# Performance work log

Hardware: AMD Instinct MI355X
Metric: run time of the kernel (lower is better)

Reference implementation:

```python
import jax, jax.numpy as jnp
import numpy as np

T = 4096          # batch_size (time points)
C = 4096          # input_dims[1] == num_filters (channels/neurons)
FW = 64           # filter_width (temporal taps)


def setup_inputs() -> dict:
    key = jax.random.key(0)
    k1, k2, k3 = jax.random.split(key, 3)
    inputs = jax.random.normal(k1, (T, C), dtype=jnp.float32)
    weights = jax.random.uniform(k2, (FW, C), dtype=jnp.float32)
    biases = jax.random.normal(k3, (C,), dtype=jnp.float32) * 0.01
    return {"inputs": inputs, "weights": weights, "biases": biases}


def reference(inputs, weights, biases):
    # weight-norm (normalize_weights=1): per-filter L2 over taps, floored at 1e-8
    wnorms = jnp.maximum(jnp.sqrt(jnp.sum(jnp.square(weights), axis=0)), 1e-8)  # [C]
    filt = jnp.maximum(0.0, weights / wnorms)  # pos_constraint clamp, [FW, C]
    # Original does a full conv2d -> [C, T, 1, C] then takes the diagonal over
    # (batch-channel, filter-channel). Mathematically this is a per-channel
    # depthwise temporal SAME conv (cross-correlation, matching tf.nn.conv2d).
    x = inputs.T[None, :, :]            # [1, C, T]  (NCH)
    k = filt.T[:, None, :]              # [C, 1, FW] (OIH), group size 1
    pre = jax.lax.conv_general_dilated(
        x, k, window_strides=(1,), padding="SAME",
        feature_group_count=C,
        dimension_numbers=("NCH", "OIH", "NCH"))  # [1, C, T]
    # bias add; activation 'lin' = identity; ei_mask is None (num_inh=0)
    out = pre[0].T + biases[None, :]    # [T, C]
    return out
```

## Files before the change

### kernel.cpp

```cpp
#include <hip/hip_runtime.h>


#define T_DIM 4096
#define C_DIM 4096
#define PAD_L 31
#define HT    32
#define KTILE 128
#define NPER  (KTILE / 32)

template <bool GUARD>
__device__ __forceinline__ void fir_body(const float* __restrict__ x,
                                         const float* __restrict__ w,
                                         const float* __restrict__ b,
                                         float* __restrict__ out,
                                         int c, int half, int t0) {
    const float* __restrict__ xp = x + c;
    const float* __restrict__ wp = w + half * HT * C_DIM + c;
    float* __restrict__ opl = out + ((long long)t0 + half) * C_DIM + c;

    float wf[HT];
    float ss = 0.0f;
#pragma unroll
    for (int j = 0; j < HT; ++j) {
        wf[j] = wp[j * C_DIM];
        ss = fmaf(wf[j], wf[j], ss);
    }
    ss += __shfl_xor(ss, 32);
    const float inv = 1.0f / fmaxf(sqrtf(ss), 1e-8f);
#pragma unroll
    for (int j = 0; j < HT; ++j) wf[j] = fmaxf(wf[j] * inv, 0.0f);

    const float bv = b[c];
    const float se = (half == 0) ? bv : 0.0f;
    const float so = (half == 0) ? 0.0f : bv;

    const int base = t0 - PAD_L + HT * half;

    float xbuf[HT];
#pragma unroll
    for (int i = 0; i < HT; ++i) {
        const int m = base + i;
        float v = 0.0f;
        if (!GUARD || ((unsigned)m < (unsigned)T_DIM)) v = xp[(long long)m * C_DIM];
        xbuf[(1 + i) & 31] = v;
    }

    float pfA[16], pfB[16];
#pragma unroll
    for (int i = 0; i < 16; ++i) {
        const int m = base + 32 + i;
        float v = 0.0f;
        if (!GUARD || ((unsigned)m < (unsigned)T_DIM)) v = xp[(long long)m * C_DIM];
        pfA[i] = v;
    }
#pragma unroll
    for (int i = 0; i < 16; ++i) {
        const int m = base + 48 + i;
        float v = 0.0f;
        if (!GUARD || ((unsigned)m < (unsigned)T_DIM)) v = xp[(long long)m * C_DIM];
        pfB[i] = v;
    }

#define PARTIAL(kk, seed, dst)                                                \
    float dst;                                                                \
    {                                                                         \
        float a0 = (seed), a1 = 0.0f;                                         \
        _Pragma("unroll")                                                     \
        for (int j = 0; j < HT; j += 2) {                                     \
            a0 = fmaf(wf[j],     xbuf[((kk) + j + 1) & 31], a0);              \
            a1 = fmaf(wf[j + 1], xbuf[((kk) + j + 2) & 31], a1);              \
        }                                                                     \
        dst = a0 + a1;                                                        \
    }

#define STEP_PAIR(kk)                                                         \
    {                                                                         \
        PARTIAL(kk, se, pe)                                                   \
        xbuf[((kk) + 1) & 31] = ((kk) < 16) ? pfA[(kk) & 15] : pfB[(kk) & 15];\
        PARTIAL((kk) + 1, so, po)                                             \
        xbuf[((kk) + 2) & 31] =                                               \
            (((kk) + 1) < 16) ? pfA[((kk) + 1) & 15] : pfB[((kk) + 1) & 15];  \
        const float snd = (half == 0) ? po : pe;                              \
        const float rcv = __shfl_xor(snd, 32);                                \
        const float res = ((half == 0) ? pe : po) + rcv;                      \
        __builtin_nontemporal_store(res, opl + (long long)(kb + (kk)) * C_DIM);\
    }

#pragma unroll 1
    for (int p = 0; p < NPER; ++p) {
        const int kb = p * 32;
        STEP_PAIR(0)  STEP_PAIR(2)  STEP_PAIR(4)  STEP_PAIR(6)
        STEP_PAIR(8)  STEP_PAIR(10) STEP_PAIR(12) STEP_PAIR(14)
        if (p < NPER - 1) {
#pragma unroll
            for (int i = 0; i < 16; ++i) {
                const int m = base + 64 + kb + i;
                float v = 0.0f;
                if (!GUARD || ((unsigned)m < (unsigned)T_DIM)) v = xp[(long long)m * C_DIM];
                pfA[i] = v;
            }
        }
        STEP_PAIR(16) STEP_PAIR(18) STEP_PAIR(20) STEP_PAIR(22)
        STEP_PAIR(24) STEP_PAIR(26) STEP_PAIR(28) STEP_PAIR(30)
        if (p < NPER - 1) {
#pragma unroll
            for (int i = 0; i < 16; ++i) {
                const int m = base + 80 + kb + i;
                float v = 0.0f;
                if (!GUARD || ((unsigned)m < (unsigned)T_DIM)) v = xp[(long long)m * C_DIM];
                pfB[i] = v;
            }
        }
    }

#undef STEP_PAIR
#undef PARTIAL
}

__global__ __launch_bounds__(256)
__attribute__((amdgpu_waves_per_eu(3, 4)))
void depthwise_fir_kernel(const float* __restrict__ x, const float* __restrict__ w,
                          const float* __restrict__ b, float* __restrict__ out) {
    const int lane = threadIdx.x & 63;
    const int wave = threadIdx.x >> 6;
    const int c    = blockIdx.y * 128 + wave * 32 + (lane & 31);
    const int half = lane >> 5;
    const int t0   = blockIdx.x * KTILE;
    if (blockIdx.x == 0 || blockIdx.x == gridDim.x - 1)
        fir_body<true>(x, w, b, out, c, half, t0);
    else
        fir_body<false>(x, w, b, out, c, half, t0);
}

extern "C" void kernel_launch(void* const* d_in, const int* in_sizes, int n_in,
                              void* d_out, int out_size, void* d_ws, size_t ws_size,
                              hipStream_t stream) {
    const float* x = (const float*)d_in[0];
    const float* w = (const float*)d_in[1];
    const float* b = (const float*)d_in[2];
    float* out = (float*)d_out;

    dim3 grid(T_DIM / KTILE, C_DIM / 128);
    dim3 block(256);
    hipLaunchKernelGGL(depthwise_fir_kernel, grid, block, 0, stream, x, w, b, out);
}
```

Measured before the change: 50.38 us.

## Split filter taps across four lane groups to cut per-thread registers

Each filter's 64 taps are now split across four 16-lane groups instead of two 32-lane halves. Each thread holds 16 weights and a 16-entry input ring buffer, and partial sums are combined with two cross-lane shuffles per output. A wave now covers 16 channels instead of 32, the grid doubles along channels, and the waves-per-EU hint is removed. The aim is lower register pressure and higher occupancy, at the cost of more shuffles per output and narrower 64-byte row segments per load and store, which may hurt coalescing.

New measurement: 61.75 us. 1.23x slower.

```diff
diff --git a/kernel.cpp b/kernel.cpp
--- a/kernel.cpp
+++ b/kernel.cpp
@@ -4,108 +4,102 @@
 #define T_DIM 4096
 #define C_DIM 4096
 #define PAD_L 31
-#define HT    32
+#define QT    16
 #define KTILE 128
-#define NPER  (KTILE / 32)
+#define NPER  (KTILE / 16)
 
 template <bool GUARD>
 __device__ __forceinline__ void fir_body(const float* __restrict__ x,
                                          const float* __restrict__ w,
                                          const float* __restrict__ b,
                                          float* __restrict__ out,
-                                         int c, int half, int t0) {
+                                         int c, int grp, int t0) {
     const float* __restrict__ xp = x + c;
-    const float* __restrict__ wp = w + half * HT * C_DIM + c;
-    float* __restrict__ opl = out + ((long long)t0 + half) * C_DIM + c;
+    const float* __restrict__ wp = w + grp * QT * C_DIM + c;
 
-    float wf[HT];
+    float wf[QT];
     float ss = 0.0f;
 #pragma unroll
-    for (int j = 0; j < HT; ++j) {
+    for (int j = 0; j < QT; ++j) {
         wf[j] = wp[j * C_DIM];
         ss = fmaf(wf[j], wf[j], ss);
     }
+    ss += __shfl_xor(ss, 16);
     ss += __shfl_xor(ss, 32);
     const float inv = 1.0f / fmaxf(sqrtf(ss), 1e-8f);
 #pragma unroll
-    for (int j = 0; j < HT; ++j) wf[j] = fmaxf(wf[j] * inv, 0.0f);
+    for (int j = 0; j < QT; ++j) wf[j] = fmaxf(wf[j] * inv, 0.0f);
 
-    const float bv = b[c];
-    const float se = (half == 0) ? bv : 0.0f;
-    const float so = (half == 0) ? 0.0f : bv;
+    const float seed = (grp == 0) ? b[c] : 0.0f;
 
-    const int base = t0 - PAD_L + HT * half;
+    const int base = t0 - PAD_L + QT * grp;
 
-    float xbuf[HT];
+    float xbuf[QT];
 #pragma unroll
-    for (int i = 0; i < HT; ++i) {
+    for (int i = 0; i < QT; ++i) {
         const int m = base + i;
         float v = 0.0f;
         if (!GUARD || ((unsigned)m < (unsigned)T_DIM)) v = xp[(long long)m * C_DIM];
-        xbuf[(1 + i) & 31] = v;
+        xbuf[(1 + i) & 15] = v;
     }
 
-    float pfA[16], pfB[16];
+    float pfA[8], pfB[8];
 #pragma unroll
-    for (int i = 0; i < 16; ++i) {
-        const int m = base + 32 + i;
+    for (int i = 0; i < 8; ++i) {
+        const int m = base + QT + i;
         float v = 0.0f;
         if (!GUARD || ((unsigned)m < (unsigned)T_DIM)) v = xp[(long long)m * C_DIM];
         pfA[i] = v;
     }
 #pragma unroll
-    for (int i = 0; i < 16; ++i) {
-        const int m = base + 48 + i;
+    for (int i = 0; i < 8; ++i) {
+        const int m = base + QT + 8 + i;
         float v = 0.0f;
         if (!GUARD || ((unsigned)m < (unsigned)T_DIM)) v = xp[(long long)m * C_DIM];
         pfB[i] = v;
     }
 
-#define PARTIAL(kk, seed, dst)                                                \
-    float dst;                                                                \
+    float res = 0.0f;
+    float* __restrict__ opl = out + ((long long)t0 + grp) * C_DIM + c;
+
+#define FIR_STEP(kk, src)                                                     \
     {                                                                         \
-        float a0 = (seed), a1 = 0.0f;                                         \
+        float a0 = seed, a1 = 0.0f;                                           \
         _Pragma("unroll")                                                     \
-        for (int j = 0; j < HT; j += 2) {                                     \
-            a0 = fmaf(wf[j],     xbuf[((kk) + j + 1) & 31], a0);              \
-            a1 = fmaf(wf[j + 1], xbuf[((kk) + j + 2) & 31], a1);              \
+        for (int j = 0; j < QT; j += 2) {                                     \
+            a0 = fmaf(wf[j],     xbuf[((kk) + j + 1) & 15], a0);              \
+            a1 = fmaf(wf[j + 1], xbuf[((kk) + j + 2) & 15], a1);              \
         }                                                                     \
-        dst = a0 + a1;                                                        \
-    }
-
-#define STEP_PAIR(kk)                                                         \
-    {                                                                         \
-        PARTIAL(kk, se, pe)                                                   \
-        xbuf[((kk) + 1) & 31] = ((kk) < 16) ? pfA[(kk) & 15] : pfB[(kk) & 15];\
-        PARTIAL((kk) + 1, so, po)                                             \
-        xbuf[((kk) + 2) & 31] =                                               \
-            (((kk) + 1) < 16) ? pfA[((kk) + 1) & 15] : pfB[((kk) + 1) & 15];  \
-        const float snd = (half == 0) ? po : pe;                              \
-        const float rcv = __shfl_xor(snd, 32);                                \
-        const float res = ((half == 0) ? pe : po) + rcv;                      \
-        __builtin_nontemporal_store(res, opl + (long long)(kb + (kk)) * C_DIM);\
+        xbuf[((kk) + 1) & 15] = src[(kk) & 7];                                \
+        float p1 = a0 + a1;                                                   \
+        p1 += __shfl_xor(p1, 16);                                             \
+        p1 += __shfl_xor(p1, 32);          \
+        res = (grp == ((kk) & 3)) ? p1 : res;     \
+        if (((kk) & 3) == 3)              \
+            __builtin_nontemporal_store(res,                                  \
+                opl + (long long)(kb + (kk) - 3) * C_DIM);                    \
     }
 
 #pragma unroll 1
     for (int p = 0; p < NPER; ++p) {
-        const int kb = p * 32;
-        STEP_PAIR(0)  STEP_PAIR(2)  STEP_PAIR(4)  STEP_PAIR(6)
-        STEP_PAIR(8)  STEP_PAIR(10) STEP_PAIR(12) STEP_PAIR(14)
+        const int kb = p * 16;
+        FIR_STEP(0, pfA)  FIR_STEP(1, pfA)  FIR_STEP(2, pfA)  FIR_STEP(3, pfA)
+        FIR_STEP(4, pfA)  FIR_STEP(5, pfA)  FIR_STEP(6, pfA)  FIR_STEP(7, pfA)
         if (p < NPER - 1) {
 #pragma unroll
-            for (int i = 0; i < 16; ++i) {
-                const int m = base + 64 + kb + i;
+            for (int i = 0; i < 8; ++i) {
+                const int m = base + kb + 32 + i;
                 float v = 0.0f;
                 if (!GUARD || ((unsigned)m < (unsigned)T_DIM)) v = xp[(long long)m * C_DIM];
                 pfA[i] = v;
             }
         }
-        STEP_PAIR(16) STEP_PAIR(18) STEP_PAIR(20) STEP_PAIR(22)
-        STEP_PAIR(24) STEP_PAIR(26) STEP_PAIR(28) STEP_PAIR(30)
+        FIR_STEP(8, pfB)  FIR_STEP(9, pfB)  FIR_STEP(10, pfB) FIR_STEP(11, pfB)
+        FIR_STEP(12, pfB) FIR_STEP(13, pfB) FIR_STEP(14, pfB) FIR_STEP(15, pfB)
         if (p < NPER - 1) {
 #pragma unroll
-            for (int i = 0; i < 16; ++i) {
-                const int m = base + 80 + kb + i;
+            for (int i = 0; i < 8; ++i) {
+                const int m = base + kb + 40 + i;
                 float v = 0.0f;
                 if (!GUARD || ((unsigned)m < (unsigned)T_DIM)) v = xp[(long long)m * C_DIM];
                 pfB[i] = v;
@@ -113,23 +107,21 @@
         }
     }
 
-#undef STEP_PAIR
-#undef PARTIAL
+#undef FIR_STEP
 }
 
-__global__ __launch_bounds__(256)
-__attribute__((amdgpu_waves_per_eu(3, 4)))
-void depthwise_fir_kernel(const float* __restrict__ x, const float* __restrict__ w,
-                          const float* __restrict__ b, float* __restrict__ out) {
+__global__ __launch_bounds__(256) void depthwise_fir_kernel(
+    const float* __restrict__ x, const float* __restrict__ w,
+    const float* __restrict__ b, float* __restrict__ out) {
     const int lane = threadIdx.x & 63;
     const int wave = threadIdx.x >> 6;
-    const int c    = blockIdx.y * 128 + wave * 32 + (lane & 31);
-    const int half = lane >> 5;
+    const int grp  = lane >> 4;
+    const int c    = blockIdx.y * 64 + wave * 16 + (lane & 15);
     const int t0   = blockIdx.x * KTILE;
     if (blockIdx.x == 0 || blockIdx.x == gridDim.x - 1)
-        fir_body<true>(x, w, b, out, c, half, t0);
+        fir_body<true>(x, w, b, out, c, grp, t0);
     else
-        fir_body<false>(x, w, b, out, c, half, t0);
+        fir_body<false>(x, w, b, out, c, grp, t0);
 }
 
 extern "C" void kernel_launch(void* const* d_in, const int* in_sizes, int n_in,
@@ -140,7 +132,7 @@
     const float* b = (const float*)d_in[2];
     float* out = (float*)d_out;
 
-    dim3 grid(T_DIM / KTILE, C_DIM / 128);
+    dim3 grid(T_DIM / KTILE, C_DIM / 64);
     dim3 block(256);
     hipLaunchKernelGGL(depthwise_fir_kernel, grid, block, 0, stream, x, w, b, out);
 }
```
